# Optimization experiments

Measured on AMD Instinct MI355X. Metric: run time of the kernel, lower is better.

Reference implementation:

```python
import jax, jax.numpy as jnp
import numpy as np

H_GRID = 512
W_GRID = 512
N_NODES = H_GRID * W_GRID


def gcn_conv(x, W, b, src, dst, n):
    # PyG GCNConv: linear transform, add self-loops, symmetric normalization,
    # scatter-add aggregation, bias.
    h = x @ W  # [N, F_out]
    # degree including self-loop (edge weights are all 1)
    deg = jax.ops.segment_sum(jnp.ones(src.shape[0], x.dtype), dst, num_segments=n) + 1.0
    dinv = jax.lax.rsqrt(deg)  # deg^-0.5
    norm = dinv[src] * dinv[dst]  # [E]
    msg = h[src] * norm[:, None]  # [E, F_out] gathered messages
    agg = jax.ops.segment_sum(msg, dst, num_segments=n)
    # self-loop contribution: norm_ii = deg_i^-0.5 * deg_i^-0.5 = 1/deg_i
    agg = agg + h * (dinv * dinv)[:, None]
    return agg + b


def setup_inputs() -> dict:
    key = jax.random.key(0)
    k_x, k_w1, k_w2, k_wfc = jax.random.split(key, 4)

    # 4-neighbor grid edges (both directions), matching build_grid_edges
    ii, jj = np.meshgrid(np.arange(H_GRID), np.arange(W_GRID), indexing='ij')
    idx = (ii * W_GRID + jj).astype(np.int32)
    src_h, dst_h = idx[:, :-1].ravel(), idx[:, 1:].ravel()
    src_v, dst_v = idx[:-1, :].ravel(), idx[1:, :].ravel()
    src = np.concatenate([src_h, dst_h, src_v, dst_v])
    dst = np.concatenate([dst_h, src_h, dst_v, src_v])
    edge_index = jnp.asarray(np.stack([src, dst]), dtype=jnp.int32)  # [2, E]

    x = jax.random.normal(k_x, (N_NODES, 2), dtype=jnp.float32)
    s1 = 1.0 / np.sqrt(2.0)
    s2 = 1.0 / np.sqrt(64.0)
    W1 = jax.random.uniform(k_w1, (2, 64), jnp.float32, -s1, s1)
    b1 = jnp.zeros((64,), jnp.float32)
    W2 = jax.random.uniform(k_w2, (64, 64), jnp.float32, -s2, s2)
    b2 = jnp.zeros((64,), jnp.float32)
    Wfc = jax.random.uniform(k_wfc, (64, 1), jnp.float32, -s2, s2)
    bfc = jnp.zeros((1,), jnp.float32)
    return {"x": x, "edge_index": edge_index, "W1": W1, "b1": b1,
            "W2": W2, "b2": b2, "Wfc": Wfc, "bfc": bfc}


def reference(x, edge_index, W1, b1, W2, b2, Wfc, bfc):
    src, dst = edge_index[0], edge_index[1]
    n = x.shape[0]
    h = jax.nn.relu(gcn_conv(x, W1, b1, src, dst, n))
    h = jax.nn.relu(gcn_conv(h, W2, b2, src, dst, n))
    out = jax.nn.sigmoid(h @ Wfc + bfc)  # [N, 1]
    return out.squeeze(-1)  # [N]
```

## Files before the change

kernel.cpp:

```cpp
#include <hip/hip_runtime.h>
#include <hip/hip_fp16.h>
#include <math.h>

#define HG 512
#define WG 512
#define TS 16
#define HS 18
#define HN (HS * HS)

typedef _Float16 f16x8 __attribute__((ext_vector_type(8)));
typedef __fp16 fp16x2 __attribute__((ext_vector_type(2)));
typedef float f32x4 __attribute__((ext_vector_type(4)));

__device__ __forceinline__ float dinv_of(int r, int c) {
    int nb = (r > 0) + (r < HG - 1) + (c > 0) + (c < WG - 1);
    return nb == 4 ? 0.4472135954999579f : (nb == 3 ? 0.5f : 0.5773502691896258f);
}

__device__ __forceinline__ int swz(int row, int ch) {
    int key = (row ^ (row >> 3)) & 7;
    return row * 128 + ((ch ^ key) << 4);
}

__device__ __forceinline__ __half2 bch2(unsigned u) { return __builtin_bit_cast(__half2, u); }
__device__ __forceinline__ unsigned pkrtz(float a, float b) {
    fp16x2 p = __builtin_amdgcn_cvt_pkrtz(a, b);
    return __builtin_bit_cast(unsigned, p);
}

__global__ __launch_bounds__(1024, 8) void fused(const float* __restrict__ x,
                                                 const float* __restrict__ W1,
                                                 const float* __restrict__ b1,
                                                 const float* __restrict__ W2,
                                                 const float* __restrict__ b2,
                                                 const float* __restrict__ Wfc,
                                                 const float* __restrict__ bfc,
                                                 float* __restrict__ out) {
    __shared__ unsigned short Hs[HN * 64];
    __shared__ unsigned short WT[64 * 64];
    __shared__ float2 a1s[HN];

    char* hb = (char*)Hs;
    char* wb = (char*)WT;
    int tid = threadIdx.x;
    int tr = blockIdx.x >> 5, tc = blockIdx.x & 31;
    int r0 = tr << 4, c0 = tc << 4;
    bool interior = (tr > 0) & (tr < 31) & (tc > 0) & (tc < 31);

    int wn = tid & 63, wkq = tid >> 6;
    float w2a = W2[(wkq * 4 + 0) * 64 + wn];
    float w2b = W2[(wkq * 4 + 1) * 64 + wn];
    float w2c = W2[(wkq * 4 + 2) * 64 + wn];
    float w2d = W2[(wkq * 4 + 3) * 64 + wn];
    int col = tid & 15;
    float b2r[4], wfr[4];
    #pragma unroll
    for (int nt = 0; nt < 4; nt++) { b2r[nt] = b2[nt * 16 + col]; wfr[nt] = Wfc[nt * 16 + col]; }
    float bfc0 = bfc[0];
    int fq = tid & 15;
    float4 w0 = ((const float4*)W1)[fq];
    float4 w1 = ((const float4*)(W1 + 64))[fq];
    float4 bb = ((const float4*)b1)[fq];

    const float2* xv = (const float2*)x;
    if (tid < HN) {
        int node = tid;
        int lr = (node * 57) >> 10;
        int lc = node - lr * 18;
        int rT = r0 - 1 + lr, cT = c0 - 1 + lc;
        float s0, s1;
        if (interior) {
            int n = (rT << 9) + cT;
            float2 vc = xv[n], vl = xv[n - 1], vr = xv[n + 1], vu = xv[n - WG], vd = xv[n + WG];
            s0 = 0.2f * (((vc.x + vl.x) + (vr.x + vu.x)) + vd.x);
            s1 = 0.2f * (((vc.y + vl.y) + (vr.y + vu.y)) + vd.y);
        } else {
            s0 = 0.f; s1 = 0.f;
            if (rT >= 0 && rT < HG && cT >= 0 && cT < WG) {
                int n = (rT << 9) + cT;
                float di = dinv_of(rT, cT);
                float2 v = xv[n];
                s0 = di * di * v.x; s1 = di * di * v.y;
                if (cT > 0)      { float w = di * dinv_of(rT, cT - 1); float2 t = xv[n - 1];  s0 += w * t.x; s1 += w * t.y; }
                if (cT < WG - 1) { float w = di * dinv_of(rT, cT + 1); float2 t = xv[n + 1];  s0 += w * t.x; s1 += w * t.y; }
                if (rT > 0)      { float w = di * dinv_of(rT - 1, cT); float2 t = xv[n - WG]; s0 += w * t.x; s1 += w * t.y; }
                if (rT < HG - 1) { float w = di * dinv_of(rT + 1, cT); float2 t = xv[n + WG]; s0 += w * t.x; s1 += w * t.y; }
            }
        }
        a1s[node] = make_float2(s0, s1);
    }

    {
        uint2 pk;
        pk.x = pkrtz(w2a, w2b);
        pk.y = pkrtz(w2c, w2d);
        *(uint2*)(wb + swz(wn, wkq >> 1) + (wkq & 1) * 8) = pk;
    }
    __syncthreads();

    for (int node = (tid >> 4); node < HN; node += 64) {
        float2 a = a1s[node];
        float h0 = fmaxf(fmaf(a.x, w0.x, fmaf(a.y, w1.x, bb.x)), 0.f);
        float h1v = fmaxf(fmaf(a.x, w0.y, fmaf(a.y, w1.y, bb.y)), 0.f);
        float h2 = fmaxf(fmaf(a.x, w0.z, fmaf(a.y, w1.z, bb.z)), 0.f);
        float h3 = fmaxf(fmaf(a.x, w0.w, fmaf(a.y, w1.w, bb.w)), 0.f);
        uint2 pk;
        pk.x = pkrtz(h0, h1v);
        pk.y = pkrtz(h2, h3);
        *(uint2*)(hb + swz(node, fq >> 1) + (fq & 1) * 8) = pk;
    }
    __syncthreads();

    int wv = tid >> 6, l = tid & 63;
    int q = l >> 4;
    int rT = r0 + wv, cT = c0 + col;
    __half2 wc2, wl2, wr2, wu2, wd2;
    if (interior) {
        wc2 = wl2 = wr2 = wu2 = wd2 = __half2half2(__float2half(0.2f));
    } else {
        float di = dinv_of(rT, cT);
        wc2 = __half2half2(__float2half(di * di));
        wl2 = __half2half2(__float2half((cT > 0)      ? di * dinv_of(rT, cT - 1) : 0.f));
        wr2 = __half2half2(__float2half((cT < WG - 1) ? di * dinv_of(rT, cT + 1) : 0.f));
        wu2 = __half2half2(__float2half((rT > 0)      ? di * dinv_of(rT - 1, cT) : 0.f));
        wd2 = __half2half2(__float2half((rT < HG - 1) ? di * dinv_of(rT + 1, cT) : 0.f));
    }
    int hrow = (wv + 1) * HS + (col + 1);

    f16x8 af[2];
    #pragma unroll
    for (int ck = 0; ck < 2; ck++) {
        int c = ck * 4 + q;
        uint4 vc = *(const uint4*)(hb + swz(hrow, c));
        uint4 vl = *(const uint4*)(hb + swz(hrow - 1, c));
        uint4 vr = *(const uint4*)(hb + swz(hrow + 1, c));
        uint4 vu = *(const uint4*)(hb + swz(hrow - HS, c));
        uint4 vd = *(const uint4*)(hb + swz(hrow + HS, c));
        const unsigned* ac = (const unsigned*)&vc;
        const unsigned* al = (const unsigned*)&vl;
        const unsigned* ar = (const unsigned*)&vr;
        const unsigned* au = (const unsigned*)&vu;
        const unsigned* ad = (const unsigned*)&vd;
        unsigned res[4];
        #pragma unroll
        for (int u = 0; u < 4; u++) {
            __half2 a = __hmul2(bch2(ac[u]), wc2);
            a = __hfma2(bch2(al[u]), wl2, a);
            a = __hfma2(bch2(ar[u]), wr2, a);
            a = __hfma2(bch2(au[u]), wu2, a);
            a = __hfma2(bch2(ad[u]), wd2, a);
            res[u] = __builtin_bit_cast(unsigned, a);
        }
        uint4 r4 = {res[0], res[1], res[2], res[3]};
        af[ck] = __builtin_bit_cast(f16x8, r4);
    }

    float p[4] = {0.f, 0.f, 0.f, 0.f};
    #pragma unroll
    for (int nt = 0; nt < 4; nt++) {
        f16x8 bf0 = *(const f16x8*)(wb + swz(nt * 16 + col, q));
        f16x8 bf1 = *(const f16x8*)(wb + swz(nt * 16 + col, 4 + q));
        f32x4 z = {0.f, 0.f, 0.f, 0.f};
        z = __builtin_amdgcn_mfma_f32_16x16x32_f16(af[0], bf0, z, 0, 0, 0);
        z = __builtin_amdgcn_mfma_f32_16x16x32_f16(af[1], bf1, z, 0, 0, 0);
        #pragma unroll
        for (int rg = 0; rg < 4; rg++)
            p[rg] += fmaxf(z[rg] + b2r[nt], 0.f) * wfr[nt];
    }
    #pragma unroll
    for (int rg = 0; rg < 4; rg++) {
        #pragma unroll
        for (int s = 1; s < 16; s <<= 1)
            p[rg] += __shfl_xor(p[rg], s, 64);
    }
    if (col == 0) {
        float4 o;
        o.x = 1.f / (1.f + __expf(-(p[0] + bfc0)));
        o.y = 1.f / (1.f + __expf(-(p[1] + bfc0)));
        o.z = 1.f / (1.f + __expf(-(p[2] + bfc0)));
        o.w = 1.f / (1.f + __expf(-(p[3] + bfc0)));
        *(float4*)&out[(rT << 9) + c0 + (q << 2)] = o;
    }
}

extern "C" void kernel_launch(void* const* d_in, const int* in_sizes, int n_in,
                              void* d_out, int out_size, void* d_ws, size_t ws_size,
                              hipStream_t stream) {
    const float* x   = (const float*)d_in[0];
    const float* W1  = (const float*)d_in[2];
    const float* b1  = (const float*)d_in[3];
    const float* W2  = (const float*)d_in[4];
    const float* b2  = (const float*)d_in[5];
    const float* Wfc = (const float*)d_in[6];
    const float* bfc = (const float*)d_in[7];
    float* out = (float*)d_out;

    fused<<<(HG / TS) * (WG / TS), 1024, 0, stream>>>(x, W1, b1, W2, b2, Wfc, bfc, out);
}
```

Measured before the change: 85.78 us.

## Precompute fp16 W2 transpose in a prep kernel and read B fragments from global

```diff
diff --git a/kernel.cpp b/kernel.cpp
--- a/kernel.cpp
+++ b/kernel.cpp
@@ -28,45 +28,56 @@
     return __builtin_bit_cast(unsigned, p);
 }
 
+__global__ __launch_bounds__(256) void prep(const float* __restrict__ W2,
+                                            unsigned short* __restrict__ wt) {
+    int t = threadIdx.x;
+    #pragma unroll
+    for (int rep = 0; rep < 2; rep++) {
+        int i = t + rep * 256;
+        int n = i >> 3, c = i & 7;
+        unsigned pk[4];
+        #pragma unroll
+        for (int j = 0; j < 4; j++) {
+            float a = W2[(c * 8 + 2 * j) * 64 + n];
+            float b = W2[(c * 8 + 2 * j + 1) * 64 + n];
+            pk[j] = pkrtz(a, b);
+        }
+        uint4 v = {pk[0], pk[1], pk[2], pk[3]};
+        ((uint4*)wt)[i] = v;
+    }
+}
+
 __global__ __launch_bounds__(1024, 8) void fused(const float* __restrict__ x,
                                                  const float* __restrict__ W1,
                                                  const float* __restrict__ b1,
-                                                 const float* __restrict__ W2,
+                                                 const unsigned short* __restrict__ wt,
                                                  const float* __restrict__ b2,
                                                  const float* __restrict__ Wfc,
                                                  const float* __restrict__ bfc,
                                                  float* __restrict__ out) {
     __shared__ unsigned short Hs[HN * 64];
-    __shared__ unsigned short WT[64 * 64];
     __shared__ float2 a1s[HN];
 
     char* hb = (char*)Hs;
-    char* wb = (char*)WT;
     int tid = threadIdx.x;
     int tr = blockIdx.x >> 5, tc = blockIdx.x & 31;
     int r0 = tr << 4, c0 = tc << 4;
     bool interior = (tr > 0) & (tr < 31) & (tc > 0) & (tc < 31);
 
-    int wn = tid & 63, wkq = tid >> 6;
-    float w2a = W2[(wkq * 4 + 0) * 64 + wn];
-    float w2b = W2[(wkq * 4 + 1) * 64 + wn];
-    float w2c = W2[(wkq * 4 + 2) * 64 + wn];
-    float w2d = W2[(wkq * 4 + 3) * 64 + wn];
     int col = tid & 15;
     float b2r[4], wfr[4];
     #pragma unroll
     for (int nt = 0; nt < 4; nt++) { b2r[nt] = b2[nt * 16 + col]; wfr[nt] = Wfc[nt * 16 + col]; }
     float bfc0 = bfc[0];
-    int fq = tid & 15;
+    int fq = col;
     float4 w0 = ((const float4*)W1)[fq];
     float4 w1 = ((const float4*)(W1 + 64))[fq];
     float4 bb = ((const float4*)b1)[fq];
 
     const float2* xv = (const float2*)x;
     if (tid < HN) {
-        int node = tid;
-        int lr = (node * 57) >> 10;
-        int lc = node - lr * 18;
+        int lr = (tid * 57) >> 10;
+        int lc = tid - lr * 18;
         int rT = r0 - 1 + lr, cT = c0 - 1 + lc;
         float s0, s1;
         if (interior) {
@@ -87,14 +98,7 @@
                 if (rT < HG - 1) { float w = di * dinv_of(rT + 1, cT); float2 t = xv[n + WG]; s0 += w * t.x; s1 += w * t.y; }
             }
         }
-        a1s[node] = make_float2(s0, s1);
-    }
-
-    {
-        uint2 pk;
-        pk.x = pkrtz(w2a, w2b);
-        pk.y = pkrtz(w2c, w2d);
-        *(uint2*)(wb + swz(wn, wkq >> 1) + (wkq & 1) * 8) = pk;
+        a1s[tid] = make_float2(s0, s1);
     }
     __syncthreads();
 
@@ -155,30 +159,33 @@
         af[ck] = __builtin_bit_cast(f16x8, r4);
     }
 
-    float p[4] = {0.f, 0.f, 0.f, 0.f};
+    float p4[4] = {0.f, 0.f, 0.f, 0.f};
     #pragma unroll
     for (int nt = 0; nt < 4; nt++) {
-        f16x8 bf0 = *(const f16x8*)(wb + swz(nt * 16 + col, q));
-        f16x8 bf1 = *(const f16x8*)(wb + swz(nt * 16 + col, 4 + q));
-        f32x4 z = {0.f, 0.f, 0.f, 0.f};
+        const unsigned short* wrow = wt + (nt * 16 + col) * 64;
+        f16x8 bf0 = *(const f16x8*)(wrow + q * 8);
+        f16x8 bf1 = *(const f16x8*)(wrow + 32 + q * 8);
+        float b2v = b2r[nt];
+        f32x4 z = {b2v, b2v, b2v, b2v};
         z = __builtin_amdgcn_mfma_f32_16x16x32_f16(af[0], bf0, z, 0, 0, 0);
         z = __builtin_amdgcn_mfma_f32_16x16x32_f16(af[1], bf1, z, 0, 0, 0);
+        float wfv = wfr[nt];
         #pragma unroll
         for (int rg = 0; rg < 4; rg++)
-            p[rg] += fmaxf(z[rg] + b2r[nt], 0.f) * wfr[nt];
+            p4[rg] += fmaxf(z[rg], 0.f) * wfv;
     }
     #pragma unroll
     for (int rg = 0; rg < 4; rg++) {
         #pragma unroll
         for (int s = 1; s < 16; s <<= 1)
-            p[rg] += __shfl_xor(p[rg], s, 64);
+            p4[rg] += __shfl_xor(p4[rg], s, 64);
     }
     if (col == 0) {
         float4 o;
-        o.x = 1.f / (1.f + __expf(-(p[0] + bfc0)));
-        o.y = 1.f / (1.f + __expf(-(p[1] + bfc0)));
-        o.z = 1.f / (1.f + __expf(-(p[2] + bfc0)));
-        o.w = 1.f / (1.f + __expf(-(p[3] + bfc0)));
+        o.x = 1.f / (1.f + __expf(-(p4[0] + bfc0)));
+        o.y = 1.f / (1.f + __expf(-(p4[1] + bfc0)));
+        o.z = 1.f / (1.f + __expf(-(p4[2] + bfc0)));
+        o.w = 1.f / (1.f + __expf(-(p4[3] + bfc0)));
         *(float4*)&out[(rT << 9) + c0 + (q << 2)] = o;
     }
 }
@@ -194,6 +201,8 @@
     const float* Wfc = (const float*)d_in[6];
     const float* bfc = (const float*)d_in[7];
     float* out = (float*)d_out;
-
-    fused<<<(HG / TS) * (WG / TS), 1024, 0, stream>>>(x, W1, b1, W2, b2, Wfc, bfc, out);
-}
+    unsigned short* wt = (unsigned short*)d_ws;
+
+    prep<<<1, 256, 0, stream>>>(W2, wt);
+    fused<<<(HG / TS) * (WG / TS), 1024, 0, stream>>>(x, W1, b1, wt, b2, Wfc, bfc, out);
+}
```

Result: slower. 94.36 us (+10.0%).
